# Kernel optimization log

Hardware: AMD Instinct MI355X
Metric: run time of the kernel (lower is better)

The kernel has to match this reference:

```python
import jax, jax.numpy as jnp
import numpy as np

NEG_INF = float('-inf')


def setup_inputs() -> dict:
    key = jax.random.key(0)
    kq, kk, kv, km = jax.random.split(key, 4)
    B, H, S, D = 2, 16, 2048, 64
    q = jax.random.normal(kq, (B, H, S, D), dtype=jnp.float32)
    k = jax.random.normal(kk, (B, H, S, D), dtype=jnp.float32)
    v = jax.random.normal(kv, (B, H, S, D), dtype=jnp.float32)
    mask = jax.random.randint(km, (B, 1, S, S), 0, 2).astype(jnp.bool_)
    return {"q": q, "k": k, "v": v, "mask": mask}


def reference(q, k, v, mask):
    d_k = q.shape[-1]
    scale = d_k ** (-0.5)
    # scores: [B,H,S,S]
    scores = jnp.einsum('bhqd,bhkd->bhqk', q, k)
    scores = jnp.where(mask, NEG_INF, scores)
    attn = jax.nn.softmax(scale * scores, axis=-1)
    return jnp.einsum('bhqk,bhkd->bhqd', attn, v)
```

## Files before the change

### kernel.cpp

```cpp
#include <hip/hip_runtime.h>


typedef __attribute__((ext_vector_type(8))) short  short8;
typedef __attribute__((ext_vector_type(4))) float  floatx4;

constexpr int   B_  = 2, H_ = 16, S_ = 2048, D_ = 64;
constexpr int   BH_ = B_ * H_;
constexpr int   KB_ = 32;
constexpr int   NT_ = S_ / KB_;
constexpr float SCALE_   = 0.125f;
constexpr float MASKVAL_ = -1e30f;
constexpr float MCLAMP_  = -1e29f;

__device__ __forceinline__ unsigned short f2bf(float f) {
  union { float f; unsigned u; } v; v.f = f;
  unsigned r = v.u + 0x7fffu + ((v.u >> 16) & 1u);
  return (unsigned short)(r >> 16);
}
__device__ __forceinline__ unsigned pk2(float lo, float hi) {
  return (unsigned)f2bf(lo) | ((unsigned)f2bf(hi) << 16);
}

__global__ __launch_bounds__(256) void prep_kernel(
    const float* __restrict__ k, const float* __restrict__ v,
    uint4* __restrict__ kimg, uint4* __restrict__ vimg) {
  int blk = blockIdx.x;
  int tid = threadIdx.x;
  int half = BH_ * NT_;
  if (blk < half) {
    int bh = blk / NT_, kt = blk % NT_;
    int krow = tid >> 3, d08 = tid & 7;
    const float* src = k + ((size_t)bh * S_ + (size_t)kt * KB_ + krow) * D_ + d08 * 8;
    float4 f0 = *(const float4*)src;
    float4 f1 = *(const float4*)(src + 4);
    uint4 w;
    w.x = pk2(f0.x, f0.y); w.y = pk2(f0.z, f0.w);
    w.z = pk2(f1.x, f1.y); w.w = pk2(f1.z, f1.w);
    int slot = d08 ^ (krow & 7);
    kimg[(size_t)blk * 256 + krow * 8 + slot] = w;
  } else {
    int blk2 = blk - half;
    int bh = blk2 / NT_, kt = blk2 % NT_;
    int d = tid & 63, k08 = tid >> 6;
    const float* src = v + ((size_t)bh * S_ + (size_t)kt * KB_ + k08 * 8) * D_ + d;
    float e[8];
#pragma unroll
    for (int j = 0; j < 8; ++j) e[j] = src[(size_t)j * D_];
    uint4 w;
    w.x = pk2(e[0], e[1]); w.y = pk2(e[2], e[3]);
    w.z = pk2(e[4], e[5]); w.w = pk2(e[6], e[7]);
    int slot = k08 ^ (d & 3);
    vimg[(size_t)blk2 * 256 + d * 4 + slot] = w;
  }
}

__global__ __launch_bounds__(256) void maskpack_kernel(
    const void* __restrict__ mask, unsigned* __restrict__ bits) {
  const unsigned* mw = (const unsigned*)mask;
  bool is_bytes = false;
#pragma unroll
  for (int i = 0; i < 16; ++i) is_bytes |= (mw[i] > 1u);

  size_t gid = (size_t)blockIdx.x * 256 + threadIdx.x;
  unsigned v = is_bytes ? (unsigned)((const unsigned char*)mask)[gid]
                        : ((const unsigned*)mask)[gid];
  unsigned long long bal = __ballot(v != 0u);
  if ((threadIdx.x & 63) == 0) {
    size_t w = gid >> 5;
    *(uint2*)&bits[w] = make_uint2((unsigned)bal, (unsigned)(bal >> 32));
  }
}

template <bool USE_BITS>
__global__ __launch_bounds__(256) void attn_kernel(
    const float* __restrict__ q, const unsigned* __restrict__ mbits,
    const void* __restrict__ mask_raw,
    const uint4* __restrict__ kimg, const uint4* __restrict__ vimg,
    float* __restrict__ out) {
  __shared__ uint4 KtL[256];
  __shared__ uint4 VtL[256];
  __shared__ __align__(16) short Pb[4 * 640];

  const int tid  = threadIdx.x;
  const int wid  = tid >> 6;
  const int lane = tid & 63;
  const int lq   = lane & 15;
  const int g    = lane >> 4;
  const int bid  = blockIdx.x;
  const int bh   = bid >> 5;
  const int qt   = bid & 31;
  const int b    = bh >> 4;

  const int qrow = qt * 64 + wid * 16 + lq;
  const float* qp = q + ((size_t)bh * S_ + qrow) * D_;

  bool is_bytes = false;
  if (!USE_BITS) {
    const unsigned* mw0 = (const unsigned*)mask_raw;
#pragma unroll
    for (int i = 0; i < 16; ++i) is_bytes |= (mw0[i] > 1u);
  }

  short8 qf[2];
#pragma unroll
  for (int t = 0; t < 2; ++t) {
    float4 f0 = *(const float4*)(qp + 8 * g + 32 * t);
    float4 f1 = *(const float4*)(qp + 8 * g + 32 * t + 4);
    short8 s;
    s[0] = (short)f2bf(f0.x); s[1] = (short)f2bf(f0.y);
    s[2] = (short)f2bf(f0.z); s[3] = (short)f2bf(f0.w);
    s[4] = (short)f2bf(f1.x); s[5] = (short)f2bf(f1.y);
    s[6] = (short)f2bf(f1.z); s[7] = (short)f2bf(f1.w);
    qf[t] = s;
  }

  const unsigned* mrow = mbits + ((size_t)b * S_ + qrow) * (size_t)NT_;
  const size_t mask_row_off = ((size_t)b * S_ + qrow) * (size_t)S_;

  float m_run = -1e30f, l_run = 0.0f;
  floatx4 acc[4];
#pragma unroll
  for (int c = 0; c < 4; ++c) acc[c] = (floatx4){0.f, 0.f, 0.f, 0.f};

  const size_t imgbase = (size_t)bh * NT_ * 256;

  KtL[tid] = kimg[imgbase + tid];
  VtL[tid] = vimg[imgbase + tid];
  __syncthreads();

  char* ldsK = (char*)KtL;
  char* ldsV = (char*)VtL;
  char* ldsP = (char*)Pb + wid * 1280 + lq * 80;

  for (int t = 0; t < NT_; ++t) {
    uint4 kn, vn;
    if (t + 1 < NT_) {
      kn = kimg[imgbase + (size_t)(t + 1) * 256 + tid];
      vn = vimg[imgbase + (size_t)(t + 1) * 256 + tid];
    }
    const int kb = t * KB_;

    unsigned mlo, mhi;
    if (USE_BITS) {
      unsigned mw = mrow[t];
      mlo = mw >> (4 * g);
      mhi = mw >> (16 + 4 * g);
    } else if (!is_bytes) {
      const unsigned* m32 = (const unsigned*)mask_raw + mask_row_off;
      uint4 a = *(const uint4*)(m32 + kb + 4 * g);
      uint4 c = *(const uint4*)(m32 + kb + 16 + 4 * g);
      mlo = (a.x ? 1u : 0u) | (a.y ? 2u : 0u) | (a.z ? 4u : 0u) | (a.w ? 8u : 0u);
      mhi = (c.x ? 1u : 0u) | (c.y ? 2u : 0u) | (c.z ? 4u : 0u) | (c.w ? 8u : 0u);
    } else {
      const unsigned char* m8 = (const unsigned char*)mask_raw + mask_row_off;
      uchar4 a = *(const uchar4*)(m8 + kb + 4 * g);
      uchar4 c = *(const uchar4*)(m8 + kb + 16 + 4 * g);
      mlo = (a.x ? 1u : 0u) | (a.y ? 2u : 0u) | (a.z ? 4u : 0u) | (a.w ? 8u : 0u);
      mhi = (c.x ? 1u : 0u) | (c.y ? 2u : 0u) | (c.z ? 4u : 0u) | (c.w ? 8u : 0u);
    }

    floatx4 c0 = (floatx4){0.f, 0.f, 0.f, 0.f};
    floatx4 c1 = (floatx4){0.f, 0.f, 0.f, 0.f};
#pragma unroll
    for (int tt = 0; tt < 2; ++tt) {
      const int sw = ((g + 4 * tt) ^ (lq & 7)) << 4;
      short8 a0 = *(const short8*)(ldsK + (size_t)lq * 128 + sw);
      short8 a1 = *(const short8*)(ldsK + (size_t)(16 + lq) * 128 + sw);
      c0 = __builtin_amdgcn_mfma_f32_16x16x32_bf16(a0, qf[tt], c0, 0, 0, 0);
      c1 = __builtin_amdgcn_mfma_f32_16x16x32_bf16(a1, qf[tt], c1, 0, 0, 0);
    }

    float s0 = (mlo & 1u) ? MASKVAL_ : c0[0] * SCALE_;
    float s1 = (mlo & 2u) ? MASKVAL_ : c0[1] * SCALE_;
    float s2 = (mlo & 4u) ? MASKVAL_ : c0[2] * SCALE_;
    float s3 = (mlo & 8u) ? MASKVAL_ : c0[3] * SCALE_;
    float s4 = (mhi & 1u) ? MASKVAL_ : c1[0] * SCALE_;
    float s5 = (mhi & 2u) ? MASKVAL_ : c1[1] * SCALE_;
    float s6 = (mhi & 4u) ? MASKVAL_ : c1[2] * SCALE_;
    float s7 = (mhi & 8u) ? MASKVAL_ : c1[3] * SCALE_;

    float tm = fmaxf(fmaxf(fmaxf(s0, s1), fmaxf(s2, s3)),
                     fmaxf(fmaxf(s4, s5), fmaxf(s6, s7)));
    tm = fmaxf(tm, __shfl_xor(tm, 16));
    tm = fmaxf(tm, __shfl_xor(tm, 32));
    float m_new = fmaxf(m_run, tm);
    float mu = fmaxf(m_new, MCLAMP_);
    float corr = __expf(fmaxf(m_run, MCLAMP_) - mu);
    float p0 = __expf(s0 - mu), p1 = __expf(s1 - mu);
    float p2 = __expf(s2 - mu), p3 = __expf(s3 - mu);
    float p4 = __expf(s4 - mu), p5 = __expf(s5 - mu);
    float p6 = __expf(s6 - mu), p7 = __expf(s7 - mu);
    float ts = ((p0 + p1) + (p2 + p3)) + ((p4 + p5) + (p6 + p7));
    ts += __shfl_xor(ts, 16);
    ts += __shfl_xor(ts, 32);
    l_run = l_run * corr + ts;
    m_run = m_new;

    *(uint2*)(ldsP + 8 * g)      = make_uint2(pk2(p0, p1), pk2(p2, p3));
    *(uint2*)(ldsP + 32 + 8 * g) = make_uint2(pk2(p4, p5), pk2(p6, p7));
    asm volatile("s_waitcnt lgkmcnt(0)" ::: "memory");
    __builtin_amdgcn_sched_barrier(0);
    short8 pa = *(const short8*)(ldsP + 16 * g);

    float cr0 = __shfl(corr, 4 * g + 0);
    float cr1 = __shfl(corr, 4 * g + 1);
    float cr2 = __shfl(corr, 4 * g + 2);
    float cr3 = __shfl(corr, 4 * g + 3);
#pragma unroll
    for (int c = 0; c < 4; ++c) {
      floatx4 a = acc[c];
      a[0] *= cr0; a[1] *= cr1; a[2] *= cr2; a[3] *= cr3;
      acc[c] = a;
    }

#pragma unroll
    for (int c = 0; c < 4; ++c) {
      short8 vb = *(const short8*)(ldsV + (size_t)(16 * c + lq) * 64 +
                                   (((g ^ (lq & 3))) << 4));
      acc[c] = __builtin_amdgcn_mfma_f32_16x16x32_bf16(pa, vb, acc[c], 0, 0, 0);
    }

    __syncthreads();
    if (t + 1 < NT_) { KtL[tid] = kn; VtL[tid] = vn; }
    __syncthreads();
  }

  float li0 = __shfl(l_run, 4 * g + 0);
  float li1 = __shfl(l_run, 4 * g + 1);
  float li2 = __shfl(l_run, 4 * g + 2);
  float li3 = __shfl(l_run, 4 * g + 3);
  float r0 = 1.0f / li0, r1 = 1.0f / li1, r2 = 1.0f / li2, r3 = 1.0f / li3;
  float* op = out + ((size_t)bh * S_ + (size_t)qt * 64 + wid * 16) * D_;
#pragma unroll
  for (int c = 0; c < 4; ++c) {
    op[(size_t)(4 * g + 0) * D_ + 16 * c + lq] = acc[c][0] * r0;
    op[(size_t)(4 * g + 1) * D_ + 16 * c + lq] = acc[c][1] * r1;
    op[(size_t)(4 * g + 2) * D_ + 16 * c + lq] = acc[c][2] * r2;
    op[(size_t)(4 * g + 3) * D_ + 16 * c + lq] = acc[c][3] * r3;
  }
}

extern "C" void kernel_launch(void* const* d_in, const int* in_sizes, int n_in,
                              void* d_out, int out_size, void* d_ws, size_t ws_size,
                              hipStream_t stream) {
  const float* q = (const float*)d_in[0];
  const float* k = (const float*)d_in[1];
  const float* v = (const float*)d_in[2];
  const void*  mask = d_in[3];

  constexpr size_t IMG_BYTES  = (size_t)BH_ * S_ * D_ * 2;
  constexpr size_t BITS_BYTES = (size_t)B_ * S_ * (S_ / 8);

  uint4*    kimg = (uint4*)d_ws;
  uint4*    vimg = (uint4*)((char*)d_ws + IMG_BYTES);
  unsigned* bits = (unsigned*)((char*)d_ws + 2 * IMG_BYTES);

  prep_kernel<<<2 * BH_ * NT_, 256, 0, stream>>>(k, v, kimg, vimg);

  if (ws_size >= 2 * IMG_BYTES + BITS_BYTES) {
    maskpack_kernel<<<(B_ * S_ * S_) / 256, 256, 0, stream>>>(mask, bits);
    attn_kernel<true><<<BH_ * 32, 256, 0, stream>>>(q, bits, mask, kimg, vimg,
                                                    (float*)d_out);
  } else {
    attn_kernel<false><<<BH_ * 32, 256, 0, stream>>>(q, bits, mask, kimg, vimg,
                                                     (float*)d_out);
  }
}
```

Before: 224.1 us.

## Double-buffer K/V tiles, defer softmax rescale, fuse mask packing into prep

Several changes land together. The K/V shared-memory tiles are double-buffered, which removes one barrier per iteration. The online-softmax rescale of the accumulator is skipped unless some row max exceeds the running max by more than a threshold, and the score scale is folded into Q. The mask-packing kernel is merged into the prep kernel to save a launch, and bf16 packing now uses the hardware v_cvt_pk instruction. The V LDS swizzle is also changed to reduce bank conflicts. Costs are doubled LDS use and a wave-wide vote branch, and deferring the rescale relies on exp staying bounded when scores exceed the stale max by up to the threshold.

```diff
diff --git a/kernel.cpp b/kernel.cpp
--- a/kernel.cpp
+++ b/kernel.cpp
@@ -11,6 +11,7 @@
 constexpr float SCALE_   = 0.125f;
 constexpr float MASKVAL_ = -1e30f;
 constexpr float MCLAMP_  = -1e29f;
+constexpr float DEFER_   = 8.0f;
 
 __device__ __forceinline__ unsigned short f2bf(float f) {
   union { float f; unsigned u; } v; v.f = f;
@@ -20,13 +21,20 @@
 __device__ __forceinline__ unsigned pk2(float lo, float hi) {
   return (unsigned)f2bf(lo) | ((unsigned)f2bf(hi) << 16);
 }
+__device__ __forceinline__ unsigned cvtpk(float lo, float hi) {
+  unsigned r;
+  asm("v_cvt_pk_bf16_f32 %0, %1, %2" : "=v"(r) : "v"(lo), "v"(hi));
+  return r;
+}
 
 __global__ __launch_bounds__(256) void prep_kernel(
     const float* __restrict__ k, const float* __restrict__ v,
-    uint4* __restrict__ kimg, uint4* __restrict__ vimg) {
+    const void* __restrict__ mask,
+    uint4* __restrict__ kimg, uint4* __restrict__ vimg,
+    unsigned* __restrict__ bits) {
   int blk = blockIdx.x;
   int tid = threadIdx.x;
-  int half = BH_ * NT_;
+  constexpr int half = BH_ * NT_;
   if (blk < half) {
     int bh = blk / NT_, kt = blk % NT_;
     int krow = tid >> 3, d08 = tid & 7;
@@ -38,7 +46,7 @@
     w.z = pk2(f1.x, f1.y); w.w = pk2(f1.z, f1.w);
     int slot = d08 ^ (krow & 7);
     kimg[(size_t)blk * 256 + krow * 8 + slot] = w;
-  } else {
+  } else if (blk < 2 * half) {
     int blk2 = blk - half;
     int bh = blk2 / NT_, kt = blk2 % NT_;
     int d = tid & 63, k08 = tid >> 6;
@@ -49,25 +57,21 @@
     uint4 w;
     w.x = pk2(e[0], e[1]); w.y = pk2(e[2], e[3]);
     w.z = pk2(e[4], e[5]); w.w = pk2(e[6], e[7]);
-    int slot = k08 ^ (d & 3);
+    int slot = k08 ^ (d & 3) ^ ((d >> 2) & 3);
     vimg[(size_t)blk2 * 256 + d * 4 + slot] = w;
-  }
-}
-
-__global__ __launch_bounds__(256) void maskpack_kernel(
-    const void* __restrict__ mask, unsigned* __restrict__ bits) {
-  const unsigned* mw = (const unsigned*)mask;
-  bool is_bytes = false;
-#pragma unroll
-  for (int i = 0; i < 16; ++i) is_bytes |= (mw[i] > 1u);
-
-  size_t gid = (size_t)blockIdx.x * 256 + threadIdx.x;
-  unsigned v = is_bytes ? (unsigned)((const unsigned char*)mask)[gid]
-                        : ((const unsigned*)mask)[gid];
-  unsigned long long bal = __ballot(v != 0u);
-  if ((threadIdx.x & 63) == 0) {
-    size_t w = gid >> 5;
-    *(uint2*)&bits[w] = make_uint2((unsigned)bal, (unsigned)(bal >> 32));
+  } else {
+    const unsigned* mw = (const unsigned*)mask;
+    bool is_bytes = false;
+#pragma unroll
+    for (int i = 0; i < 16; ++i) is_bytes |= (mw[i] > 1u);
+    size_t gid = (size_t)(blk - 2 * half) * 256 + tid;
+    unsigned vv = is_bytes ? (unsigned)((const unsigned char*)mask)[gid]
+                           : ((const unsigned*)mask)[gid];
+    unsigned long long bal = __ballot(vv != 0u);
+    if ((tid & 63) == 0) {
+      size_t w = gid >> 5;
+      *(uint2*)&bits[w] = make_uint2((unsigned)bal, (unsigned)(bal >> 32));
+    }
   }
 }
 
@@ -77,8 +81,8 @@
     const void* __restrict__ mask_raw,
     const uint4* __restrict__ kimg, const uint4* __restrict__ vimg,
     float* __restrict__ out) {
-  __shared__ uint4 KtL[256];
-  __shared__ uint4 VtL[256];
+  __shared__ uint4 KtA[256], KtB[256];
+  __shared__ uint4 VtA[256], VtB[256];
   __shared__ __align__(16) short Pb[4 * 640];
 
   const int tid  = threadIdx.x;
@@ -106,12 +110,12 @@
   for (int t = 0; t < 2; ++t) {
     float4 f0 = *(const float4*)(qp + 8 * g + 32 * t);
     float4 f1 = *(const float4*)(qp + 8 * g + 32 * t + 4);
-    short8 s;
-    s[0] = (short)f2bf(f0.x); s[1] = (short)f2bf(f0.y);
-    s[2] = (short)f2bf(f0.z); s[3] = (short)f2bf(f0.w);
-    s[4] = (short)f2bf(f1.x); s[5] = (short)f2bf(f1.y);
-    s[6] = (short)f2bf(f1.z); s[7] = (short)f2bf(f1.w);
-    qf[t] = s;
+    union { unsigned u[4]; short8 s; } cv;
+    cv.u[0] = cvtpk(f0.x * SCALE_, f0.y * SCALE_);
+    cv.u[1] = cvtpk(f0.z * SCALE_, f0.w * SCALE_);
+    cv.u[2] = cvtpk(f1.x * SCALE_, f1.y * SCALE_);
+    cv.u[3] = cvtpk(f1.z * SCALE_, f1.w * SCALE_);
+    qf[t] = cv.s;
   }
 
   const unsigned* mrow = mbits + ((size_t)b * S_ + qrow) * (size_t)NT_;
@@ -124,12 +128,12 @@
 
   const size_t imgbase = (size_t)bh * NT_ * 256;
 
-  KtL[tid] = kimg[imgbase + tid];
-  VtL[tid] = vimg[imgbase + tid];
+  KtA[tid] = kimg[imgbase + tid];
+  VtA[tid] = vimg[imgbase + tid];
   __syncthreads();
 
-  char* ldsK = (char*)KtL;
-  char* ldsV = (char*)VtL;
+  uint4* Kc = KtA; uint4* Vc = VtA;
+  uint4* Kn = KtB; uint4* Vn = VtB;
   char* ldsP = (char*)Pb + wid * 1280 + lq * 80;
 
   for (int t = 0; t < NT_; ++t) {
@@ -139,6 +143,8 @@
       vn = vimg[imgbase + (size_t)(t + 1) * 256 + tid];
     }
     const int kb = t * KB_;
+    const char* ldsK = (const char*)Kc;
+    const char* ldsV = (const char*)Vc;
 
     unsigned mlo, mhi;
     if (USE_BITS) {
@@ -170,22 +176,40 @@
       c1 = __builtin_amdgcn_mfma_f32_16x16x32_bf16(a1, qf[tt], c1, 0, 0, 0);
     }
 
-    float s0 = (mlo & 1u) ? MASKVAL_ : c0[0] * SCALE_;
-    float s1 = (mlo & 2u) ? MASKVAL_ : c0[1] * SCALE_;
-    float s2 = (mlo & 4u) ? MASKVAL_ : c0[2] * SCALE_;
-    float s3 = (mlo & 8u) ? MASKVAL_ : c0[3] * SCALE_;
-    float s4 = (mhi & 1u) ? MASKVAL_ : c1[0] * SCALE_;
-    float s5 = (mhi & 2u) ? MASKVAL_ : c1[1] * SCALE_;
-    float s6 = (mhi & 4u) ? MASKVAL_ : c1[2] * SCALE_;
-    float s7 = (mhi & 8u) ? MASKVAL_ : c1[3] * SCALE_;
+    float s0 = (mlo & 1u) ? MASKVAL_ : c0[0];
+    float s1 = (mlo & 2u) ? MASKVAL_ : c0[1];
+    float s2 = (mlo & 4u) ? MASKVAL_ : c0[2];
+    float s3 = (mlo & 8u) ? MASKVAL_ : c0[3];
+    float s4 = (mhi & 1u) ? MASKVAL_ : c1[0];
+    float s5 = (mhi & 2u) ? MASKVAL_ : c1[1];
+    float s6 = (mhi & 4u) ? MASKVAL_ : c1[2];
+    float s7 = (mhi & 8u) ? MASKVAL_ : c1[3];
 
     float tm = fmaxf(fmaxf(fmaxf(s0, s1), fmaxf(s2, s3)),
                      fmaxf(fmaxf(s4, s5), fmaxf(s6, s7)));
     tm = fmaxf(tm, __shfl_xor(tm, 16));
     tm = fmaxf(tm, __shfl_xor(tm, 32));
-    float m_new = fmaxf(m_run, tm);
-    float mu = fmaxf(m_new, MCLAMP_);
-    float corr = __expf(fmaxf(m_run, MCLAMP_) - mu);
+
+    float mu = fmaxf(m_run, MCLAMP_);
+    if (!__all(tm <= mu + DEFER_)) {
+      float m_new = fmaxf(m_run, tm);
+      float mu2 = fmaxf(m_new, MCLAMP_);
+      float corr = __expf(mu - mu2);
+      l_run *= corr;
+      float cr0 = __shfl(corr, 4 * g + 0);
+      float cr1 = __shfl(corr, 4 * g + 1);
+      float cr2 = __shfl(corr, 4 * g + 2);
+      float cr3 = __shfl(corr, 4 * g + 3);
+#pragma unroll
+      for (int c = 0; c < 4; ++c) {
+        floatx4 a = acc[c];
+        a[0] *= cr0; a[1] *= cr1; a[2] *= cr2; a[3] *= cr3;
+        acc[c] = a;
+      }
+      m_run = m_new;
+      mu = mu2;
+    }
+
     float p0 = __expf(s0 - mu), p1 = __expf(s1 - mu);
     float p2 = __expf(s2 - mu), p3 = __expf(s3 - mu);
     float p4 = __expf(s4 - mu), p5 = __expf(s5 - mu);
@@ -193,36 +217,25 @@
     float ts = ((p0 + p1) + (p2 + p3)) + ((p4 + p5) + (p6 + p7));
     ts += __shfl_xor(ts, 16);
     ts += __shfl_xor(ts, 32);
-    l_run = l_run * corr + ts;
-    m_run = m_new;
-
-    *(uint2*)(ldsP + 8 * g)      = make_uint2(pk2(p0, p1), pk2(p2, p3));
-    *(uint2*)(ldsP + 32 + 8 * g) = make_uint2(pk2(p4, p5), pk2(p6, p7));
+    l_run += ts;
+
+    *(uint2*)(ldsP + 8 * g)      = make_uint2(cvtpk(p0, p1), cvtpk(p2, p3));
+    *(uint2*)(ldsP + 32 + 8 * g) = make_uint2(cvtpk(p4, p5), cvtpk(p6, p7));
     asm volatile("s_waitcnt lgkmcnt(0)" ::: "memory");
     __builtin_amdgcn_sched_barrier(0);
     short8 pa = *(const short8*)(ldsP + 16 * g);
 
-    float cr0 = __shfl(corr, 4 * g + 0);
-    float cr1 = __shfl(corr, 4 * g + 1);
-    float cr2 = __shfl(corr, 4 * g + 2);
-    float cr3 = __shfl(corr, 4 * g + 3);
-#pragma unroll
-    for (int c = 0; c < 4; ++c) {
-      floatx4 a = acc[c];
-      a[0] *= cr0; a[1] *= cr1; a[2] *= cr2; a[3] *= cr3;
-      acc[c] = a;
-    }
-
 #pragma unroll
     for (int c = 0; c < 4; ++c) {
       short8 vb = *(const short8*)(ldsV + (size_t)(16 * c + lq) * 64 +
-                                   (((g ^ (lq & 3))) << 4));
+                                   ((g ^ (lq & 3) ^ ((lq >> 2) & 3)) << 4));
       acc[c] = __builtin_amdgcn_mfma_f32_16x16x32_bf16(pa, vb, acc[c], 0, 0, 0);
     }
 
+    if (t + 1 < NT_) { Kn[tid] = kn; Vn[tid] = vn; }
     __syncthreads();
-    if (t + 1 < NT_) { KtL[tid] = kn; VtL[tid] = vn; }
-    __syncthreads();
+    uint4* tk = Kc; Kc = Kn; Kn = tk;
+    uint4* tv = Vc; Vc = Vn; Vn = tv;
   }
 
   float li0 = __shfl(l_run, 4 * g + 0);
@@ -250,15 +263,18 @@
 
   constexpr size_t IMG_BYTES  = (size_t)BH_ * S_ * D_ * 2;
   constexpr size_t BITS_BYTES = (size_t)B_ * S_ * (S_ / 8);
+  constexpr int    PREP_BLKS  = 2 * BH_ * NT_;
+  constexpr int    MASK_BLKS  = (B_ * S_ * S_) / 256;
 
   uint4*    kimg = (uint4*)d_ws;
   uint4*    vimg = (uint4*)((char*)d_ws + IMG_BYTES);
   unsigned* bits = (unsigned*)((char*)d_ws + 2 * IMG_BYTES);
 
-  prep_kernel<<<2 * BH_ * NT_, 256, 0, stream>>>(k, v, kimg, vimg);
-
-  if (ws_size >= 2 * IMG_BYTES + BITS_BYTES) {
-    maskpack_kernel<<<(B_ * S_ * S_) / 256, 256, 0, stream>>>(mask, bits);
+  const bool use_bits = (ws_size >= 2 * IMG_BYTES + BITS_BYTES);
+  const int  grid = PREP_BLKS + (use_bits ? MASK_BLKS : 0);
+
+  prep_kernel<<<grid, 256, 0, stream>>>(k, v, mask, kimg, vimg, bits);
+  if (use_bits) {
     attn_kernel<true><<<BH_ * 32, 256, 0, stream>>>(q, bits, mask, kimg, vimg,
                                                     (float*)d_out);
   } else {
```

After: 209.6 us. 1.07x faster.
